# Kernel optimization log

Measured on AMD Instinct MI355X. Metric: run time of the kernel, lower is better.

Reference implementation:

```python
import jax, jax.numpy as jnp
import numpy as np

N_NODES = 50000
N_EDGES = 800000
LEAKY_SLOPE = 0.01
DROPOUT_P = 0.5


def _graph_conv(src, dst, x, W, b):
    """DGL GraphConv with norm='both': D_out^{-1/2} A D_in^{-1/2} X W + b."""
    n = x.shape[0]
    ones = jnp.ones((src.shape[0],), dtype=x.dtype)
    deg_out = jax.ops.segment_sum(ones, src, num_segments=n)  # out-degree of src nodes
    deg_in = jax.ops.segment_sum(ones, dst, num_segments=n)   # in-degree of dst nodes
    norm_src = jax.lax.rsqrt(jnp.maximum(deg_out, 1.0))
    norm_dst = jax.lax.rsqrt(jnp.maximum(deg_in, 1.0))
    h = (x * norm_src[:, None]) @ W          # apply weight before aggregation
    agg = jax.ops.segment_sum(h[src], dst, num_segments=n)  # SpMM aggregate
    return agg * norm_dst[:, None] + b


def _dropout(x, key, p=DROPOUT_P):
    keep = jax.random.bernoulli(key, 1.0 - p, x.shape)
    return jnp.where(keep, x / (1.0 - p), jnp.zeros((), x.dtype))


def setup_inputs() -> dict:
    key = jax.random.key(0)
    ks = jax.random.split(key, 8)
    features = jax.random.normal(ks[0], (N_NODES, 128), dtype=jnp.float32)
    src = jax.random.randint(ks[1], (N_EDGES,), 0, N_NODES, dtype=jnp.int64)
    dst = jax.random.randint(ks[2], (N_EDGES,), 0, N_NODES, dtype=jnp.int64)
    s1 = 1.0 / np.sqrt(128.0)
    s3 = 1.0 / np.sqrt(128.0)
    W1 = jax.random.normal(ks[3], (128, 128), dtype=jnp.float32) * s1
    W2 = jax.random.normal(ks[4], (128, 128), dtype=jnp.float32) * s1
    W3 = jax.random.normal(ks[5], (128, 64), dtype=jnp.float32) * s3
    b1 = jnp.zeros((128,), dtype=jnp.float32)
    b2 = jnp.zeros((128,), dtype=jnp.float32)
    b3 = jnp.zeros((64,), dtype=jnp.float32)
    return {"features": features, "src": src, "dst": dst,
            "W1": W1, "b1": b1, "W2": W2, "b2": b2, "W3": W3, "b3": b3}


def reference(features, src, dst, W1, b1, W2, b2, W3, b3):
    dk = jax.random.split(jax.random.key(42), 3)
    h = jax.nn.leaky_relu(_graph_conv(src, dst, features, W1, b1), LEAKY_SLOPE)
    h = _dropout(h, dk[0])
    h = jax.nn.leaky_relu(_graph_conv(src, dst, h, W2, b2), LEAKY_SLOPE)
    h = _dropout(h, dk[1])
    h = jax.nn.leaky_relu(_graph_conv(src, dst, h, W3, b3), LEAKY_SLOPE)
    h = _dropout(h, dk[2])
    return h
```

## Files before the change

kernel.cpp:

```cpp
#include <hip/hip_runtime.h>
#include <hip/hip_fp16.h>
#include <stdint.h>

using half8 = __attribute__((ext_vector_type(8))) _Float16;
using f32x4 = __attribute__((ext_vector_type(4))) float;

#define SLOT_CAP 64
#define LDW 136
#define NBINS 50176
#define LWORDS 12544
#define NCHUNK 128

#define TFR(r) { x0 += x1; x1 = (x1 << r) | (x1 >> (32 - r)); x1 ^= x0; }

__host__ __device__ inline void threefry2x32(uint32_t k0, uint32_t k1,
                                             uint32_t c0, uint32_t c1,
                                             uint32_t& o0, uint32_t& o1) {
  uint32_t ks2 = k0 ^ k1 ^ 0x1BD11BDAu;
  uint32_t x0 = c0 + k0, x1 = c1 + k1;
  TFR(13) TFR(15) TFR(26) TFR(6)  x0 += k1;  x1 += ks2 + 1u;
  TFR(17) TFR(29) TFR(16) TFR(24) x0 += ks2; x1 += k0 + 2u;
  TFR(13) TFR(15) TFR(26) TFR(6)  x0 += k0;  x1 += k1 + 3u;
  TFR(17) TFR(29) TFR(16) TFR(24) x0 += k1;  x1 += ks2 + 4u;
  TFR(13) TFR(15) TFR(26) TFR(6)  x0 += ks2; x1 += k0 + 5u;
  o0 = x0; o1 = x1;
}

__device__ inline float tf_uniform(uint32_t k0, uint32_t k1, uint32_t i) {
  uint32_t o0, o1;
  threefry2x32(k0, k1, 0u, i, o0, o1);
  uint32_t bits = o0 ^ o1;
  return __uint_as_float((bits >> 9) | 0x3F800000u) - 1.0f;
}

__device__ inline uint16_t f2h(float f) {
  union { _Float16 h; uint16_t u; } c; c.h = (_Float16)f; return c.u;
}
__device__ inline uint32_t pack2h(float a, float b) {
  return (uint32_t)f2h(a) | ((uint32_t)f2h(b) << 16);
}
__device__ inline __half2 u2h2(uint32_t u) {
  union { uint32_t u; __half2 h; } c; c.u = u; return c.h;
}

__device__ inline void hacc(__half2* a, uint4 r) {
  a[0] = __hadd2(a[0], u2h2(r.x));
  a[1] = __hadd2(a[1], u2h2(r.y));
  a[2] = __hadd2(a[2], u2h2(r.z));
  a[3] = __hadd2(a[3], u2h2(r.w));
}

#define GDECL \
  uint4 A0, A1, A2, A3, A4, A5, A6, A7, B0, B1, B2, B3, B4, B5, B6, B7, \
        C0, C1, C2, C3, C4, C5, C6, C7, D0, D1, D2, D3, D4, D5, D6, D7;

#define GPTRS(sl, P) \
  const uint16_t* P##0 = hb + ((size_t)((sl).x & 0xFFFFu) << 7); \
  const uint16_t* P##1 = hb + ((size_t)((sl).x >> 16) << 7);     \
  const uint16_t* P##2 = hb + ((size_t)((sl).y & 0xFFFFu) << 7); \
  const uint16_t* P##3 = hb + ((size_t)((sl).y >> 16) << 7);     \
  const uint16_t* P##4 = hb + ((size_t)((sl).z & 0xFFFFu) << 7); \
  const uint16_t* P##5 = hb + ((size_t)((sl).z >> 16) << 7);     \
  const uint16_t* P##6 = hb + ((size_t)((sl).w & 0xFFFFu) << 7); \
  const uint16_t* P##7 = hb + ((size_t)((sl).w >> 16) << 7);

#define GLOAD(P, X, Y) \
  X##0 = *(const uint4*)P##0; Y##0 = *(const uint4*)(P##0 + 8); \
  X##1 = *(const uint4*)P##1; Y##1 = *(const uint4*)(P##1 + 8); \
  X##2 = *(const uint4*)P##2; Y##2 = *(const uint4*)(P##2 + 8); \
  X##3 = *(const uint4*)P##3; Y##3 = *(const uint4*)(P##3 + 8); \
  X##4 = *(const uint4*)P##4; Y##4 = *(const uint4*)(P##4 + 8); \
  X##5 = *(const uint4*)P##5; Y##5 = *(const uint4*)(P##5 + 8); \
  X##6 = *(const uint4*)P##6; Y##6 = *(const uint4*)(P##6 + 8); \
  X##7 = *(const uint4*)P##7; Y##7 = *(const uint4*)(P##7 + 8);

#define GHACC(X, Y) \
  hacc(ha, X##0); hacc(ha + 4, Y##0); \
  hacc(ha, X##1); hacc(ha + 4, Y##1); \
  hacc(ha, X##2); hacc(ha + 4, Y##2); \
  hacc(ha, X##3); hacc(ha + 4, Y##3); \
  hacc(ha, X##4); hacc(ha + 4, Y##4); \
  hacc(ha, X##5); hacc(ha + 4, Y##5); \
  hacc(ha, X##6); hacc(ha + 4, Y##6); \
  hacc(ha, X##7); hacc(ha + 4, Y##7);

#define ODECL uint4 A0, A1, A2, A3, A4, A5, A6, A7, C0, C1, C2, C3, C4, C5, C6, C7;

#define OPTRS(sl, P) \
  const uint16_t* P##0 = hb + ((size_t)((sl).x & 0xFFFFu) << 6); \
  const uint16_t* P##1 = hb + ((size_t)((sl).x >> 16) << 6);     \
  const uint16_t* P##2 = hb + ((size_t)((sl).y & 0xFFFFu) << 6); \
  const uint16_t* P##3 = hb + ((size_t)((sl).y >> 16) << 6);     \
  const uint16_t* P##4 = hb + ((size_t)((sl).z & 0xFFFFu) << 6); \
  const uint16_t* P##5 = hb + ((size_t)((sl).z >> 16) << 6);     \
  const uint16_t* P##6 = hb + ((size_t)((sl).w & 0xFFFFu) << 6); \
  const uint16_t* P##7 = hb + ((size_t)((sl).w >> 16) << 6);

#define OLOAD(P, X) \
  X##0 = *(const uint4*)P##0; X##1 = *(const uint4*)P##1; \
  X##2 = *(const uint4*)P##2; X##3 = *(const uint4*)P##3; \
  X##4 = *(const uint4*)P##4; X##5 = *(const uint4*)P##5; \
  X##6 = *(const uint4*)P##6; X##7 = *(const uint4*)P##7;

#define OHACC(X) \
  hacc(ha, X##0); hacc(ha, X##1); hacc(ha, X##2); hacc(ha, X##3); \
  hacc(ha, X##4); hacc(ha, X##5); hacc(ha, X##6); hacc(ha, X##7);

__global__ __launch_bounds__(256) void build_hist_kernel(
    const int* __restrict__ src, const int* __restrict__ dst,
    uint16_t* __restrict__ histD, uint16_t* __restrict__ histS,
    const float* __restrict__ W1, const float* __restrict__ W2,
    const float* __restrict__ W3, uint16_t* __restrict__ Wt,
    uint16_t* __restrict__ edge_slots,
    int n, int nE, int HR, int EPB) {
  const int bid = (int)blockIdx.x;
  if (bid >= 672) {
    const uint32_t pk = ((uint32_t)n << 16) | (uint32_t)(n & 0xFFFF);
    uint4 f; f.x = pk; f.y = pk; f.z = pk; f.w = pk;
    uint4* es4 = (uint4*)edge_slots;
    const int total = n * (SLOT_CAP / 8);
    for (int i = (bid - 672) * 256 + (int)threadIdx.x; i < total; i += 256 * 256)
      es4[i] = f;
    return;
  }
  if (bid >= 512) {
    int i = (bid - 512) * 256 + (int)threadIdx.x;
    float v;
    if (i < 16384) {
      int nr = i >> 7, k = i & 127;
      v = W1[k * 128 + nr];
    } else if (i < 32768) {
      int j = i - 16384, nr = j >> 7, k = j & 127;
      v = W2[k * 128 + nr];
    } else if (i < 40960) {
      int j = i - 32768, nr = j >> 7, k = j & 127;
      v = W3[k * 64 + nr];
    } else return;
    Wt[i] = f2h(v);
    return;
  }

  __shared__ uint32_t bins[LWORDS];
  const bool isSrc = bid >= 256;
  const int c = bid & 127;
  const int h = (bid >> 7) & 1;
  const int lo = h * HR;
  const int* keys = isSrc ? src : dst;
  uint16_t* hist = isSrc ? histS : histD;

  for (int i = threadIdx.x; i < LWORDS; i += 256) bins[i] = 0u;
  __syncthreads();

  const int e0 = c * EPB, e1 = min(e0 + EPB, nE);
  for (int e = e0 + (int)threadIdx.x; e < e1; e += 256) {
    int k = keys[e] - lo;
    if ((unsigned)k < (unsigned)HR)
      atomicAdd(&bins[k >> 1], 1u << ((k & 1) * 16));
  }
  __syncthreads();

  uint32_t* out = (uint32_t*)(hist + (size_t)c * NBINS + lo);
  const int wlim = (min(HR, n - lo) + 1) >> 1;
  for (int i = threadIdx.x; i < wlim; i += 256) out[i] = bins[i];
}

__global__ __launch_bounds__(256) void reduce_kernel(
    uint16_t* __restrict__ histD, const uint16_t* __restrict__ histS,
    int* __restrict__ degin, float* __restrict__ nsrc, int n) {
  const int v = blockIdx.x * 256 + (int)threadIdx.x;
  if (v >= n) return;
  uint32_t run = 0;
  #pragma unroll 4
  for (int c = 0; c < NCHUNK; ++c) {
    size_t idx = (size_t)c * NBINS + v;
    uint16_t x = histD[idx];
    histD[idx] = (uint16_t)run;
    run += x;
  }
  degin[v] = (int)run;
  uint32_t s = 0;
  #pragma unroll 4
  for (int c = 0; c < NCHUNK; ++c) s += histS[(size_t)c * NBINS + v];
  nsrc[v] = rsqrtf(fmaxf((float)s, 1.0f));
}

__global__ __launch_bounds__(256) void scatter_gemm1_kernel(
    const int* __restrict__ src, const int* __restrict__ dst,
    const uint16_t* __restrict__ cumD, uint16_t* __restrict__ edge_slots,
    const float* __restrict__ X, const float* __restrict__ nsrc,
    const uint16_t* __restrict__ Wt1, uint16_t* __restrict__ h1,
    int n, int nE, int HR, int EPB) {
  __shared__ uint32_t bins[LWORDS];
  const int bid = (int)blockIdx.x;

  if (bid < 256) {
    const int c = bid & 127;
    const int h = (bid >> 7) & 1;
    const int lo = h * HR;

    for (int i = threadIdx.x; i < LWORDS; i += 256) bins[i] = 0u;
    __syncthreads();

    const int e0 = c * EPB, e1 = min(e0 + EPB, nE);
    for (int e = e0 + (int)threadIdx.x; e < e1; e += 256) {
      int d = dst[e];
      int k = d - lo;
      if ((unsigned)k < (unsigned)HR) {
        uint32_t old = atomicAdd(&bins[k >> 1], 1u << ((k & 1) * 16));
        int rank = (int)((old >> ((k & 1) * 16)) & 0xFFFFu);
        int pos = (int)cumD[(size_t)c * NBINS + d] + rank;
        if (pos < SLOT_CAP) edge_slots[((size_t)d << 6) + pos] = (uint16_t)src[e];
      }
    }
    return;
  }

  const int r0 = (bid - 256) * 64;
  const int tid = (int)threadIdx.x;
  const int wave = tid >> 6, lane = tid & 63;
  const int wm = wave & 1, wn = wave >> 1;
  const int lane15 = lane & 15, quad = lane >> 4;

  const int rowA0 = r0 + wm * 32 + lane15;
  const int rowA1 = rowA0 + 16;
  const bool v0 = rowA0 < n, v1 = rowA1 < n;

  f32x4 acc[2][4] = {};
  #pragma unroll
  for (int kc = 0; kc < 128; kc += 32) {
    const int ko = kc + quad * 8;
    half8 a0 = {}, a1 = {};
    if (v0) {
      float4 x0 = *(const float4*)&X[(size_t)rowA0 * 128 + ko];
      float4 x1 = *(const float4*)&X[(size_t)rowA0 * 128 + ko + 4];
      a0[0] = (_Float16)x0.x; a0[1] = (_Float16)x0.y;
      a0[2] = (_Float16)x0.z; a0[3] = (_Float16)x0.w;
      a0[4] = (_Float16)x1.x; a0[5] = (_Float16)x1.y;
      a0[6] = (_Float16)x1.z; a0[7] = (_Float16)x1.w;
    }
    if (v1) {
      float4 x0 = *(const float4*)&X[(size_t)rowA1 * 128 + ko];
      float4 x1 = *(const float4*)&X[(size_t)rowA1 * 128 + ko + 4];
      a1[0] = (_Float16)x0.x; a1[1] = (_Float16)x0.y;
      a1[2] = (_Float16)x0.z; a1[3] = (_Float16)x0.w;
      a1[4] = (_Float16)x1.x; a1[5] = (_Float16)x1.y;
      a1[6] = (_Float16)x1.z; a1[7] = (_Float16)x1.w;
    }
    #pragma unroll
    for (int nt = 0; nt < 4; ++nt) {
      int nn = wn * 64 + nt * 16 + lane15;
      half8 b = *(const half8*)&Wt1[nn * 128 + ko];
      acc[0][nt] = __builtin_amdgcn_mfma_f32_16x16x32_f16(a0, b, acc[0][nt], 0, 0, 0);
      acc[1][nt] = __builtin_amdgcn_mfma_f32_16x16x32_f16(a1, b, acc[1][nt], 0, 0, 0);
    }
  }

  #pragma unroll
  for (int mt = 0; mt < 2; ++mt) {
    #pragma unroll
    for (int reg = 0; reg < 4; ++reg) {
      int row = r0 + wm * 32 + mt * 16 + quad * 4 + reg;
      float nsr = (row < n) ? nsrc[row] : 0.0f;
      #pragma unroll
      for (int nt = 0; nt < 4; ++nt) {
        int col = wn * 64 + nt * 16 + lane15;
        h1[(size_t)row * 128 + col] = f2h(acc[mt][nt][reg] * nsr);
      }
    }
  }
}

template<int NCOLS>
__global__ __launch_bounds__(256, 3) void fuse_gather_gemm_kernel(
    const uint16_t* __restrict__ h_in, const int* __restrict__ degin,
    const uint16_t* __restrict__ edge_slots, const float* __restrict__ nsrc,
    const float* __restrict__ bias, const uint16_t* __restrict__ Wt,
    uint16_t* __restrict__ h_out, uint32_t k0, uint32_t k1, int n) {
  __shared__ uint16_t Xs[32 * LDW];
  __shared__ float ns_s[32];
  const int r0 = (int)blockIdx.x * 32;
  const int tid = (int)threadIdx.x;

  if (tid < 32) {
    int row = r0 + tid;
    ns_s[tid] = (row < n) ? nsrc[row] : 1.0f;
  }

  const int nl = tid >> 3;
  const int node = r0 + nl;
  const int c16 = (tid & 7) * 16;

  if (node < n) {
    __half2 ha[8];
    #pragma unroll
    for (int j = 0; j < 8; ++j) ha[j] = __half2(__float2half(0.f), __float2half(0.f));

    const int dgi = degin[node];
    const int deg = min(dgi, SLOT_CAP);
    const uint16_t* slots = edge_slots + ((size_t)node << 6);
    const uint16_t* hb = h_in + c16;
    const int nb = (deg + 7) >> 3;

    GDECL
    if (nb > 0) {
      uint4 sA = *(const uint4*)&slots[0];
      GPTRS(sA, p)
      GLOAD(p, A, B)
      int b = 1;
      for (; b + 1 < nb; b += 2) {
        uint4 sB = *(const uint4*)&slots[b * 8];
        uint4 sC = *(const uint4*)&slots[b * 8 + 8];
        GPTRS(sB, q)
        GLOAD(q, C, D)
        GHACC(A, B)
        GPTRS(sC, r)
        GLOAD(r, A, B)
        GHACC(C, D)
      }
      if (b < nb) {
        uint4 sB = *(const uint4*)&slots[b * 8];
        GPTRS(sB, q)
        GLOAD(q, C, D)
        GHACC(A, B)
        GHACC(C, D)
      } else {
        GHACC(A, B)
      }
    }

    float acc[16];
    #pragma unroll
    for (int j = 0; j < 8; ++j) {
      float2 f = __half22float2(ha[j]);
      acc[2 * j] = f.x; acc[2 * j + 1] = f.y;
    }

    const float nd = rsqrtf(fmaxf((float)dgi, 1.0f));
    const float4 b0 = *(const float4*)&bias[c16];
    const float4 b1 = *(const float4*)&bias[c16 + 4];
    const float4 b2 = *(const float4*)&bias[c16 + 8];
    const float4 b3 = *(const float4*)&bias[c16 + 12];
    const float bb[16] = {b0.x, b0.y, b0.z, b0.w, b1.x, b1.y, b1.z, b1.w,
                          b2.x, b2.y, b2.z, b2.w, b3.x, b3.y, b3.z, b3.w};
    const uint32_t i0 = (uint32_t)(node * 128 + c16);

    float o[16];
    #pragma unroll
    for (int j = 0; j < 16; ++j) {
      float v = acc[j] * nd + bb[j];
      v = (v >= 0.f) ? v : 0.01f * v;
      o[j] = (tf_uniform(k0, k1, i0 + (uint32_t)j) < 0.5f) ? v * 2.0f : 0.0f;
    }

    uint4 w0, w1;
    w0.x = pack2h(o[0], o[1]);   w0.y = pack2h(o[2], o[3]);
    w0.z = pack2h(o[4], o[5]);   w0.w = pack2h(o[6], o[7]);
    w1.x = pack2h(o[8], o[9]);   w1.y = pack2h(o[10], o[11]);
    w1.z = pack2h(o[12], o[13]); w1.w = pack2h(o[14], o[15]);
    *(uint4*)&Xs[nl * LDW + c16] = w0;
    *(uint4*)&Xs[nl * LDW + c16 + 8] = w1;
  } else {
    uint4 z = make_uint4(0u, 0u, 0u, 0u);
    *(uint4*)&Xs[nl * LDW + c16] = z;
    *(uint4*)&Xs[nl * LDW + c16 + 8] = z;
  }
  __syncthreads();

  const int wave = tid >> 6, lane = tid & 63;
  const int wm = wave & 1, wn = wave >> 1;
  const int lane15 = lane & 15, quad = lane >> 4;
  constexpr int NT = NCOLS / 32;

  f32x4 acc[NT] = {};
  #pragma unroll
  for (int kc = 0; kc < 128; kc += 32) {
    const int ko = kc + quad * 8;
    half8 a = *(const half8*)&Xs[(wm * 16 + lane15) * LDW + ko];
    #pragma unroll
    for (int nt = 0; nt < NT; ++nt) {
      int nn = wn * (NCOLS / 2) + nt * 16 + lane15;
      half8 b = *(const half8*)&Wt[nn * 128 + ko];
      acc[nt] = __builtin_amdgcn_mfma_f32_16x16x32_f16(a, b, acc[nt], 0, 0, 0);
    }
  }

  #pragma unroll
  for (int nt = 0; nt < NT; ++nt) {
    #pragma unroll
    for (int reg = 0; reg < 4; ++reg) {
      int rl = wm * 16 + quad * 4 + reg;
      int row = r0 + rl;
      int col = wn * (NCOLS / 2) + nt * 16 + lane15;
      h_out[(size_t)row * NCOLS + col] = f2h(acc[nt][reg] * ns_s[rl]);
    }
  }
}

__global__ __launch_bounds__(256, 4) void gather_out_kernel(
    const uint16_t* __restrict__ h3, const int* __restrict__ degin,
    const uint16_t* __restrict__ edge_slots, const float* __restrict__ bias,
    float* __restrict__ out, uint32_t k0, uint32_t k1, int n) {
  const int node = (int)blockIdx.x * 32 + (int)(threadIdx.x >> 3);
  if (node >= n) return;
  const int c8 = (threadIdx.x & 7) * 8;

  const int dgi = degin[node];
  const int deg = min(dgi, SLOT_CAP);
  const uint16_t* slots = edge_slots + ((size_t)node << 6);
  const uint16_t* hb = h3 + c8;
  const int nb = (deg + 7) >> 3;

  __half2 ha[4];
  #pragma unroll
  for (int j = 0; j < 4; ++j) ha[j] = __half2(__float2half(0.f), __float2half(0.f));

  ODECL
  if (nb > 0) {
    uint4 sA = *(const uint4*)&slots[0];
    OPTRS(sA, p)
    OLOAD(p, A)
    int b = 1;
    for (; b + 1 < nb; b += 2) {
      uint4 sB = *(const uint4*)&slots[b * 8];
      uint4 sC = *(const uint4*)&slots[b * 8 + 8];
      OPTRS(sB, q)
      OLOAD(q, C)
      OHACC(A)
      OPTRS(sC, r)
      OLOAD(r, A)
      OHACC(C)
    }
    if (b < nb) {
      uint4 sB = *(const uint4*)&slots[b * 8];
      OPTRS(sB, q)
      OLOAD(q, C)
      OHACC(A)
      OHACC(C)
    } else {
      OHACC(A)
    }
  }

  float acc[8];
  #pragma unroll
  for (int j = 0; j < 4; ++j) {
    float2 f = __half22float2(ha[j]);
    acc[2 * j] = f.x; acc[2 * j + 1] = f.y;
  }

  const float nd = rsqrtf(fmaxf((float)dgi, 1.0f));
  const float4 b0 = *(const float4*)&bias[c8];
  const float4 b1 = *(const float4*)&bias[c8 + 4];
  const float bb[8] = {b0.x, b0.y, b0.z, b0.w, b1.x, b1.y, b1.z, b1.w};
  const uint32_t i0 = (uint32_t)(node * 64 + c8);

  float o[8];
  #pragma unroll
  for (int j = 0; j < 8; ++j) {
    float v = acc[j] * nd + bb[j];
    v = (v >= 0.f) ? v : 0.01f * v;
    o[j] = (tf_uniform(k0, k1, i0 + (uint32_t)j) < 0.5f) ? v * 2.0f : 0.0f;
  }

  float* op = &out[(size_t)node * 64 + c8];
  *(float4*)op = make_float4(o[0], o[1], o[2], o[3]);
  *(float4*)(op + 4) = make_float4(o[4], o[5], o[6], o[7]);
}

extern "C" void kernel_launch(void* const* d_in, const int* in_sizes, int n_in,
                              void* d_out, int out_size, void* d_ws, size_t ws_size,
                              hipStream_t stream) {
  const float* features = (const float*)d_in[0];
  const int*   src      = (const int*)d_in[1];
  const int*   dst      = (const int*)d_in[2];
  const float* W1       = (const float*)d_in[3];
  const float* b1       = (const float*)d_in[4];
  const float* W2       = (const float*)d_in[5];
  const float* b2       = (const float*)d_in[6];
  const float* W3       = (const float*)d_in[7];
  const float* b3       = (const float*)d_in[8];
  float* out = (float*)d_out;

  const int n  = in_sizes[0] / 128;
  const int nE = in_sizes[1];
  const int nA = ((n + 63) / 64) * 64;

  char* p = (char*)d_ws;
  uint16_t* histD      = (uint16_t*)p; p += (size_t)NCHUNK * NBINS * 2;
  uint16_t* histS      = (uint16_t*)p; p += (size_t)NCHUNK * NBINS * 2;
  int* degin           = (int*)p;      p += (size_t)n * 4;
  float* nsrc          = (float*)p;    p += (size_t)n * 4;
  uint16_t* edge_slots = (uint16_t*)p; p += (size_t)n * SLOT_CAP * 2;
  uint16_t* Wt         = (uint16_t*)p; p += 40960 * 2;
  uint16_t* h1         = (uint16_t*)p; p += (size_t)nA * 128 * 2;
  uint16_t* h2         = (uint16_t*)p; p += (size_t)nA * 128 * 2;
  uint16_t* h3         = (uint16_t*)p;

  uint32_t dk[3][2];
  for (uint32_t i = 0; i < 3; ++i)
    threefry2x32(0u, 42u, 0u, i, dk[i][0], dk[i][1]);

  const int EPB = (nE + NCHUNK - 1) / NCHUNK;
  int HR = ((n + 3) / 2) & ~1;
  if (HR > 2 * LWORDS) HR = 2 * LWORDS;
  const int gb64 = (n + 63) / 64;
  const int gb32 = (n + 31) / 32;

  build_hist_kernel<<<928, 256, 0, stream>>>(src, dst, histD, histS,
                                             W1, W2, W3, Wt, edge_slots,
                                             n, nE, HR, EPB);
  reduce_kernel<<<(n + 255) / 256, 256, 0, stream>>>(histD, histS, degin, nsrc, n);
  scatter_gemm1_kernel<<<256 + gb64, 256, 0, stream>>>(
      src, dst, histD, edge_slots, features, nsrc, Wt, h1, n, nE, HR, EPB);
  fuse_gather_gemm_kernel<128><<<gb32, 256, 0, stream>>>(
      h1, degin, edge_slots, nsrc, b1, Wt + 16384, h2, dk[0][0], dk[0][1], n);
  fuse_gather_gemm_kernel<64><<<gb32, 256, 0, stream>>>(
      h2, degin, edge_slots, nsrc, b2, Wt + 32768, h3, dk[1][0], dk[1][1], n);
  gather_out_kernel<<<(n + 31) / 32, 256, 0, stream>>>(
      h3, degin, edge_slots, b3, out, dk[2][0], dk[2][1], n);
}
```

Baseline: 248.7 us.

## Replace chunked LDS histograms with direct global-atomic edge scatter

The graph preprocessing used per-chunk LDS histograms, a prefix-sum reduce over 128 chunk histograms and a second LDS pass to place each edge in its destination's slot list. This replaces all of that with one grid-stride kernel that does global atomicAdd on per-destination counters to claim slots and on per-source out-degree counters. The source normalisation is recomputed inline from the degree where it is used. This drops two large histogram buffers and a kernel launch, but the order of edges within a slot list now depends on atomic timing rather than being fixed, and global atomics on random addresses can contend.

Result: slower. 280.4 us (+12.8%).

```diff
diff --git a/kernel.cpp b/kernel.cpp
--- a/kernel.cpp
+++ b/kernel.cpp
@@ -7,9 +7,6 @@
 
 #define SLOT_CAP 64
 #define LDW 136
-#define NBINS 50176
-#define LWORDS 12544
-#define NCHUNK 128
 
 #define TFR(r) { x0 += x1; x1 = (x1 << r) | (x1 >> (32 - r)); x1 ^= x0; }
 
@@ -106,25 +103,22 @@
   hacc(ha, X##0); hacc(ha, X##1); hacc(ha, X##2); hacc(ha, X##3); \
   hacc(ha, X##4); hacc(ha, X##5); hacc(ha, X##6); hacc(ha, X##7);
 
-__global__ __launch_bounds__(256) void build_hist_kernel(
-    const int* __restrict__ src, const int* __restrict__ dst,
-    uint16_t* __restrict__ histD, uint16_t* __restrict__ histS,
+__global__ __launch_bounds__(256) void init_kernel(
     const float* __restrict__ W1, const float* __restrict__ W2,
     const float* __restrict__ W3, uint16_t* __restrict__ Wt,
-    uint16_t* __restrict__ edge_slots,
-    int n, int nE, int HR, int EPB) {
+    uint16_t* __restrict__ edge_slots, uint32_t* __restrict__ cnt2,
+    int n) {
+  const int fb = (n * 8 + 255) >> 8;
   const int bid = (int)blockIdx.x;
-  if (bid >= 672) {
+  if (bid < fb) {
     const uint32_t pk = ((uint32_t)n << 16) | (uint32_t)(n & 0xFFFF);
     uint4 f; f.x = pk; f.y = pk; f.z = pk; f.w = pk;
-    uint4* es4 = (uint4*)edge_slots;
-    const int total = n * (SLOT_CAP / 8);
-    for (int i = (bid - 672) * 256 + (int)threadIdx.x; i < total; i += 256 * 256)
-      es4[i] = f;
+    const int i = bid * 256 + (int)threadIdx.x;
+    if (i < n * 8) ((uint4*)edge_slots)[i] = f;
     return;
   }
-  if (bid >= 512) {
-    int i = (bid - 512) * 256 + (int)threadIdx.x;
+  if (bid < fb + 160) {
+    int i = (bid - fb) * 256 + (int)threadIdx.x;
     float v;
     if (i < 16384) {
       int nr = i >> 7, k = i & 127;
@@ -139,83 +133,28 @@
     Wt[i] = f2h(v);
     return;
   }
-
-  __shared__ uint32_t bins[LWORDS];
-  const bool isSrc = bid >= 256;
-  const int c = bid & 127;
-  const int h = (bid >> 7) & 1;
-  const int lo = h * HR;
-  const int* keys = isSrc ? src : dst;
-  uint16_t* hist = isSrc ? histS : histD;
-
-  for (int i = threadIdx.x; i < LWORDS; i += 256) bins[i] = 0u;
-  __syncthreads();
-
-  const int e0 = c * EPB, e1 = min(e0 + EPB, nE);
-  for (int e = e0 + (int)threadIdx.x; e < e1; e += 256) {
-    int k = keys[e] - lo;
-    if ((unsigned)k < (unsigned)HR)
-      atomicAdd(&bins[k >> 1], 1u << ((k & 1) * 16));
-  }
-  __syncthreads();
-
-  uint32_t* out = (uint32_t*)(hist + (size_t)c * NBINS + lo);
-  const int wlim = (min(HR, n - lo) + 1) >> 1;
-  for (int i = threadIdx.x; i < wlim; i += 256) out[i] = bins[i];
-}
-
-__global__ __launch_bounds__(256) void reduce_kernel(
-    uint16_t* __restrict__ histD, const uint16_t* __restrict__ histS,
-    int* __restrict__ degin, float* __restrict__ nsrc, int n) {
-  const int v = blockIdx.x * 256 + (int)threadIdx.x;
-  if (v >= n) return;
-  uint32_t run = 0;
-  #pragma unroll 4
-  for (int c = 0; c < NCHUNK; ++c) {
-    size_t idx = (size_t)c * NBINS + v;
-    uint16_t x = histD[idx];
-    histD[idx] = (uint16_t)run;
-    run += x;
-  }
-  degin[v] = (int)run;
-  uint32_t s = 0;
-  #pragma unroll 4
-  for (int c = 0; c < NCHUNK; ++c) s += histS[(size_t)c * NBINS + v];
-  nsrc[v] = rsqrtf(fmaxf((float)s, 1.0f));
-}
-
-__global__ __launch_bounds__(256) void scatter_gemm1_kernel(
+  const int i = (bid - fb - 160) * 256 + (int)threadIdx.x;
+  if (i < 2 * n) cnt2[i] = 0u;
+}
+
+__global__ __launch_bounds__(256) void edge_scatter_kernel(
     const int* __restrict__ src, const int* __restrict__ dst,
-    const uint16_t* __restrict__ cumD, uint16_t* __restrict__ edge_slots,
-    const float* __restrict__ X, const float* __restrict__ nsrc,
-    const uint16_t* __restrict__ Wt1, uint16_t* __restrict__ h1,
-    int n, int nE, int HR, int EPB) {
-  __shared__ uint32_t bins[LWORDS];
-  const int bid = (int)blockIdx.x;
-
-  if (bid < 256) {
-    const int c = bid & 127;
-    const int h = (bid >> 7) & 1;
-    const int lo = h * HR;
-
-    for (int i = threadIdx.x; i < LWORDS; i += 256) bins[i] = 0u;
-    __syncthreads();
-
-    const int e0 = c * EPB, e1 = min(e0 + EPB, nE);
-    for (int e = e0 + (int)threadIdx.x; e < e1; e += 256) {
-      int d = dst[e];
-      int k = d - lo;
-      if ((unsigned)k < (unsigned)HR) {
-        uint32_t old = atomicAdd(&bins[k >> 1], 1u << ((k & 1) * 16));
-        int rank = (int)((old >> ((k & 1) * 16)) & 0xFFFFu);
-        int pos = (int)cumD[(size_t)c * NBINS + d] + rank;
-        if (pos < SLOT_CAP) edge_slots[((size_t)d << 6) + pos] = (uint16_t)src[e];
-      }
-    }
-    return;
-  }
-
-  const int r0 = (bid - 256) * 64;
+    uint16_t* __restrict__ edge_slots, int* __restrict__ cnt,
+    int* __restrict__ degS, int nE) {
+  const int stride = (int)gridDim.x * 256;
+  for (int e = (int)blockIdx.x * 256 + (int)threadIdx.x; e < nE; e += stride) {
+    const int d = dst[e];
+    const int s = src[e];
+    atomicAdd(&degS[s], 1);
+    const int pos = atomicAdd(&cnt[d], 1);
+    if (pos < SLOT_CAP) edge_slots[((size_t)d << 6) + pos] = (uint16_t)s;
+  }
+}
+
+__global__ __launch_bounds__(256) void gemm1_kernel(
+    const float* __restrict__ X, const int* __restrict__ degS,
+    const uint16_t* __restrict__ Wt1, uint16_t* __restrict__ h1, int n) {
+  const int r0 = (int)blockIdx.x * 64;
   const int tid = (int)threadIdx.x;
   const int wave = tid >> 6, lane = tid & 63;
   const int wm = wave & 1, wn = wave >> 1;
@@ -260,7 +199,7 @@
     #pragma unroll
     for (int reg = 0; reg < 4; ++reg) {
       int row = r0 + wm * 32 + mt * 16 + quad * 4 + reg;
-      float nsr = (row < n) ? nsrc[row] : 0.0f;
+      float nsr = (row < n) ? rsqrtf(fmaxf((float)degS[row], 1.0f)) : 0.0f;
       #pragma unroll
       for (int nt = 0; nt < 4; ++nt) {
         int col = wn * 64 + nt * 16 + lane15;
@@ -273,7 +212,7 @@
 template<int NCOLS>
 __global__ __launch_bounds__(256, 3) void fuse_gather_gemm_kernel(
     const uint16_t* __restrict__ h_in, const int* __restrict__ degin,
-    const uint16_t* __restrict__ edge_slots, const float* __restrict__ nsrc,
+    const uint16_t* __restrict__ edge_slots, const int* __restrict__ degS,
     const float* __restrict__ bias, const uint16_t* __restrict__ Wt,
     uint16_t* __restrict__ h_out, uint32_t k0, uint32_t k1, int n) {
   __shared__ uint16_t Xs[32 * LDW];
@@ -283,7 +222,7 @@
 
   if (tid < 32) {
     int row = r0 + tid;
-    ns_s[tid] = (row < n) ? nsrc[row] : 1.0f;
+    ns_s[tid] = (row < n) ? rsqrtf(fmaxf((float)degS[row], 1.0f)) : 1.0f;
   }
 
   const int nl = tid >> 3;
@@ -486,10 +425,8 @@
   const int nA = ((n + 63) / 64) * 64;
 
   char* p = (char*)d_ws;
-  uint16_t* histD      = (uint16_t*)p; p += (size_t)NCHUNK * NBINS * 2;
-  uint16_t* histS      = (uint16_t*)p; p += (size_t)NCHUNK * NBINS * 2;
-  int* degin           = (int*)p;      p += (size_t)n * 4;
-  float* nsrc          = (float*)p;    p += (size_t)n * 4;
+  int* cnt             = (int*)p;      p += (size_t)n * 4;
+  int* degS            = (int*)p;      p += (size_t)n * 4;
   uint16_t* edge_slots = (uint16_t*)p; p += (size_t)n * SLOT_CAP * 2;
   uint16_t* Wt         = (uint16_t*)p; p += 40960 * 2;
   uint16_t* h1         = (uint16_t*)p; p += (size_t)nA * 128 * 2;
@@ -500,22 +437,20 @@
   for (uint32_t i = 0; i < 3; ++i)
     threefry2x32(0u, 42u, 0u, i, dk[i][0], dk[i][1]);
 
-  const int EPB = (nE + NCHUNK - 1) / NCHUNK;
-  int HR = ((n + 3) / 2) & ~1;
-  if (HR > 2 * LWORDS) HR = 2 * LWORDS;
   const int gb64 = (n + 63) / 64;
   const int gb32 = (n + 31) / 32;
-
-  build_hist_kernel<<<928, 256, 0, stream>>>(src, dst, histD, histS,
-                                             W1, W2, W3, Wt, edge_slots,
-                                             n, nE, HR, EPB);
-  reduce_kernel<<<(n + 255) / 256, 256, 0, stream>>>(histD, histS, degin, nsrc, n);
-  scatter_gemm1_kernel<<<256 + gb64, 256, 0, stream>>>(
-      src, dst, histD, edge_slots, features, nsrc, Wt, h1, n, nE, HR, EPB);
+  const int fb = (n * 8 + 255) / 256;
+  const int zb = (2 * n + 255) / 256;
+
+  init_kernel<<<fb + 160 + zb, 256, 0, stream>>>(
+      W1, W2, W3, Wt, edge_slots, (uint32_t*)cnt, n);
+  edge_scatter_kernel<<<2048, 256, 0, stream>>>(
+      src, dst, edge_slots, cnt, degS, nE);
+  gemm1_kernel<<<gb64, 256, 0, stream>>>(features, degS, Wt, h1, n);
   fuse_gather_gemm_kernel<128><<<gb32, 256, 0, stream>>>(
-      h1, degin, edge_slots, nsrc, b1, Wt + 16384, h2, dk[0][0], dk[0][1], n);
+      h1, cnt, edge_slots, degS, b1, Wt + 16384, h2, dk[0][0], dk[0][1], n);
   fuse_gather_gemm_kernel<64><<<gb32, 256, 0, stream>>>(
-      h2, degin, edge_slots, nsrc, b2, Wt + 32768, h3, dk[1][0], dk[1][1], n);
-  gather_out_kernel<<<(n + 31) / 32, 256, 0, stream>>>(
-      h3, degin, edge_slots, b3, out, dk[2][0], dk[2][1], n);
-}
+      h2, cnt, edge_slots, degS, b2, Wt + 32768, h3, dk[1][0], dk[1][1], n);
+  gather_out_kernel<<<gb32, 256, 0, stream>>>(
+      h3, cnt, edge_slots, b3, out, dk[2][0], dk[2][1], n);
+}
```

## Overlap dropout RNG with gather loads and restructure gather pipelines

Applied to the files above, without the earlier changes.

In both gather kernels, the Threefry dropout random numbers are now computed right after the first one or two batches of neighbour-row loads are issued. Scheduling barriers keep that integer work in the shadow of memory latency instead of running it after aggregation. The gather loop is restructured into a two-buffer ping-pong with barriers between load and accumulate stages. Launch-bound occupancy hints are lowered so the kernels can use the extra registers for the precomputed randoms. The first slot batch is now loaded and accumulated even when a node has no in-edges, which relies on the padded slot contents being safe to read and add.

Result: slower. 253.7 us (+2.0%).

```diff
diff --git a/kernel.cpp b/kernel.cpp
--- a/kernel.cpp
+++ b/kernel.cpp
@@ -10,6 +10,7 @@
 #define NBINS 50176
 #define LWORDS 12544
 #define NCHUNK 128
+#define SBAR __builtin_amdgcn_sched_barrier(0)
 
 #define TFR(r) { x0 += x1; x1 = (x1 << r) | (x1 >> (32 - r)); x1 ^= x0; }
 
@@ -271,7 +272,7 @@
 }
 
 template<int NCOLS>
-__global__ __launch_bounds__(256, 3) void fuse_gather_gemm_kernel(
+__global__ __launch_bounds__(256, 2) void fuse_gather_gemm_kernel(
     const uint16_t* __restrict__ h_in, const int* __restrict__ degin,
     const uint16_t* __restrict__ edge_slots, const float* __restrict__ nsrc,
     const float* __restrict__ bias, const uint16_t* __restrict__ Wt,
@@ -297,35 +298,44 @@
 
     const int dgi = degin[node];
     const int deg = min(dgi, SLOT_CAP);
-    const uint16_t* slots = edge_slots + ((size_t)node << 6);
+    const uint4* slots4 = (const uint4*)(edge_slots + ((size_t)node << 6));
     const uint16_t* hb = h_in + c16;
     const int nb = (deg + 7) >> 3;
 
     GDECL
-    if (nb > 0) {
-      uint4 sA = *(const uint4*)&slots[0];
-      GPTRS(sA, p)
+    float u[16];
+    {
+      uint4 s0 = slots4[0];
+      GPTRS(s0, p)
       GLOAD(p, A, B)
-      int b = 1;
-      for (; b + 1 < nb; b += 2) {
-        uint4 sB = *(const uint4*)&slots[b * 8];
-        uint4 sC = *(const uint4*)&slots[b * 8 + 8];
-        GPTRS(sB, q)
+      if (nb > 1) {
+        uint4 s1 = slots4[1];
+        GPTRS(s1, q)
         GLOAD(q, C, D)
-        GHACC(A, B)
-        GPTRS(sC, r)
-        GLOAD(r, A, B)
+      }
+      SBAR;
+      const uint32_t i0 = (uint32_t)(node * 128 + c16);
+      #pragma unroll
+      for (int j = 0; j < 16; ++j) u[j] = tf_uniform(k0, k1, i0 + (uint32_t)j);
+      SBAR;
+
+      GHACC(A, B)
+      for (int b = 2; b < nb; b += 2) {
+        uint4 sb = slots4[b];
+        GPTRS(sb, p2)
+        GLOAD(p2, A, B)
+        SBAR;
         GHACC(C, D)
-      }
-      if (b < nb) {
-        uint4 sB = *(const uint4*)&slots[b * 8];
-        GPTRS(sB, q)
-        GLOAD(q, C, D)
-        GHACC(A, B)
-        GHACC(C, D)
-      } else {
+        SBAR;
+        if (b + 1 < nb) {
+          uint4 sc = slots4[b + 1];
+          GPTRS(sc, q2)
+          GLOAD(q2, C, D)
+          SBAR;
+        }
         GHACC(A, B)
       }
+      if ((nb > 1) && !(nb & 1)) { GHACC(C, D) }
     }
 
     float acc[16];
@@ -342,14 +352,13 @@
     const float4 b3 = *(const float4*)&bias[c16 + 12];
     const float bb[16] = {b0.x, b0.y, b0.z, b0.w, b1.x, b1.y, b1.z, b1.w,
                           b2.x, b2.y, b2.z, b2.w, b3.x, b3.y, b3.z, b3.w};
-    const uint32_t i0 = (uint32_t)(node * 128 + c16);
 
     float o[16];
     #pragma unroll
     for (int j = 0; j < 16; ++j) {
       float v = acc[j] * nd + bb[j];
       v = (v >= 0.f) ? v : 0.01f * v;
-      o[j] = (tf_uniform(k0, k1, i0 + (uint32_t)j) < 0.5f) ? v * 2.0f : 0.0f;
+      o[j] = (u[j] < 0.5f) ? v * 2.0f : 0.0f;
     }
 
     uint4 w0, w1;
@@ -396,7 +405,7 @@
   }
 }
 
-__global__ __launch_bounds__(256, 4) void gather_out_kernel(
+__global__ __launch_bounds__(256, 3) void gather_out_kernel(
     const uint16_t* __restrict__ h3, const int* __restrict__ degin,
     const uint16_t* __restrict__ edge_slots, const float* __restrict__ bias,
     float* __restrict__ out, uint32_t k0, uint32_t k1, int n) {
@@ -406,7 +415,7 @@
 
   const int dgi = degin[node];
   const int deg = min(dgi, SLOT_CAP);
-  const uint16_t* slots = edge_slots + ((size_t)node << 6);
+  const uint4* slots4 = (const uint4*)(edge_slots + ((size_t)node << 6));
   const uint16_t* hb = h3 + c8;
   const int nb = (deg + 7) >> 3;
 
@@ -415,30 +424,39 @@
   for (int j = 0; j < 4; ++j) ha[j] = __half2(__float2half(0.f), __float2half(0.f));
 
   ODECL
-  if (nb > 0) {
-    uint4 sA = *(const uint4*)&slots[0];
-    OPTRS(sA, p)
+  float u[8];
+  {
+    uint4 s0 = slots4[0];
+    OPTRS(s0, p)
     OLOAD(p, A)
-    int b = 1;
-    for (; b + 1 < nb; b += 2) {
-      uint4 sB = *(const uint4*)&slots[b * 8];
-      uint4 sC = *(const uint4*)&slots[b * 8 + 8];
-      OPTRS(sB, q)
+    if (nb > 1) {
+      uint4 s1 = slots4[1];
+      OPTRS(s1, q)
       OLOAD(q, C)
+    }
+    SBAR;
+    const uint32_t i0 = (uint32_t)(node * 64 + c8);
+    #pragma unroll
+    for (int j = 0; j < 8; ++j) u[j] = tf_uniform(k0, k1, i0 + (uint32_t)j);
+    SBAR;
+
+    OHACC(A)
+    for (int b = 2; b < nb; b += 2) {
+      uint4 sb = slots4[b];
+      OPTRS(sb, p2)
+      OLOAD(p2, A)
+      SBAR;
+      OHACC(C)
+      SBAR;
+      if (b + 1 < nb) {
+        uint4 sc = slots4[b + 1];
+        OPTRS(sc, q2)
+        OLOAD(q2, C)
+        SBAR;
+      }
       OHACC(A)
-      OPTRS(sC, r)
-      OLOAD(r, A)
-      OHACC(C)
-    }
-    if (b < nb) {
-      uint4 sB = *(const uint4*)&slots[b * 8];
-      OPTRS(sB, q)
-      OLOAD(q, C)
-      OHACC(A)
-      OHACC(C)
-    } else {
-      OHACC(A)
-    }
+    }
+    if ((nb > 1) && !(nb & 1)) { OHACC(C) }
   }
 
   float acc[8];
@@ -452,14 +470,13 @@
   const float4 b0 = *(const float4*)&bias[c8];
   const float4 b1 = *(const float4*)&bias[c8 + 4];
   const float bb[8] = {b0.x, b0.y, b0.z, b0.w, b1.x, b1.y, b1.z, b1.w};
-  const uint32_t i0 = (uint32_t)(node * 64 + c8);
 
   float o[8];
   #pragma unroll
   for (int j = 0; j < 8; ++j) {
     float v = acc[j] * nd + bb[j];
     v = (v >= 0.f) ? v : 0.01f * v;
-    o[j] = (tf_uniform(k0, k1, i0 + (uint32_t)j) < 0.5f) ? v * 2.0f : 0.0f;
+    o[j] = (u[j] < 0.5f) ? v * 2.0f : 0.0f;
   }
 
   float* op = &out[(size_t)node * 64 + c8];
@@ -516,6 +533,6 @@
       h1, degin, edge_slots, nsrc, b1, Wt + 16384, h2, dk[0][0], dk[0][1], n);
   fuse_gather_gemm_kernel<64><<<gb32, 256, 0, stream>>>(
       h2, degin, edge_slots, nsrc, b2, Wt + 32768, h3, dk[1][0], dk[1][1], n);
-  gather_out_kernel<<<(n + 31) / 32, 256, 0, stream>>>(
+  gather_out_kernel<<<gb32, 256, 0, stream>>>(
       h3, degin, edge_slots, b3, out, dk[2][0], dk[2][1], n);
 }
```
